# Kernel optimization log

Hardware: AMD Instinct MI355X
Metric: run time of the kernel (lower is better)

The kernel has to match this reference:

```python
import jax, jax.numpy as jnp
import numpy as np

H = 256    # hidden_size
CVQ = 64   # vq_ph_channel
K = 128    # vq_ph_codebook_dim
NL = 5     # num_layers per ConvBlocks
NB = 2     # layers_in_block
KS = 3     # kernel_size


def _ln_c(x, g, b, eps=1e-5):
    # LayerNorm over channel dim of a [B, C, T] tensor
    m = jnp.mean(x, axis=1, keepdims=True)
    v = jnp.mean((x - m) ** 2, axis=1, keepdims=True)
    return (x - m) * jax.lax.rsqrt(v + eps) * g[None, :, None] + b[None, :, None]


def _causal_conv(x, w, b):
    # x [B,Cin,T], w [Cout,Cin,K]; left (causal) padding of K-1
    y = jax.lax.conv_general_dilated(x, w, (1,), [(w.shape[-1] - 1, 0)],
                                     dimension_numbers=('NCH', 'OIH', 'NCH'))
    return y + b[None, :, None]


def _pw(x, w, b):
    # pointwise (kernel-size-1) conv: w [Cout, Cin]
    return jnp.einsum('oi,bit->bot', w, x) + b[None, :, None]


def _conv_blocks(x, mask, ln_g, ln_b, w1, b1, w2, b2, last_g, last_b, post_w, post_b):
    # LeftPadConvBlocks: NL residual blocks x NB sub-blocks of
    # LN -> causal conv (C->2C, k=3) -> *k^-0.5 -> GELU -> 1x1 conv (2C->C), residual + mask
    scale = KS ** -0.5
    for i in range(NL):
        for j in range(NB):
            h = _ln_c(x, ln_g[i, j], ln_b[i, j])
            h = _causal_conv(h, w1[i, j], b1[i, j]) * scale
            h = jax.nn.gelu(h, approximate=False)
            h = _pw(h, w2[i, j], b2[i, j])
            x = (x + h) * mask
    x = _ln_c(x, last_g, last_b) * mask
    x = _causal_conv(x, post_w, post_b) * mask
    return x


def _group_by_segs(h_bct, mel2ph, L):
    # scatter-mean mel frames into phoneme segments; index 0 = padding (dropped)
    h = jnp.swapaxes(h_bct, 1, 2)  # [B, T, H]
    def one(hb, mb):
        s = jnp.zeros((L + 1, hb.shape[-1]), hb.dtype).at[mb].add(hb)
        c = jnp.zeros((L + 1,), hb.dtype).at[mb].add(1.0)
        return s[1:] / jnp.clip(c[1:], 1.0)[:, None]
    g = jax.vmap(one)(h, mel2ph)   # [B, L, H]
    return jnp.swapaxes(g, 1, 2)   # [B, H, L]


def _vq(z, codebook, beta=0.25):
    # EMA-VQ forward math: nearest-codebook lookup + straight-through + commitment loss
    x = jnp.swapaxes(z, 1, 2)                                # [B, T, C]
    d = (jnp.sum(x ** 2, -1, keepdims=True)
         - 2.0 * jnp.einsum('btc,kc->btk', x, codebook)
         + jnp.sum(codebook ** 2, -1))                       # [B, T, K]
    idx = jnp.argmin(d, axis=-1)                             # [B, T]
    q = codebook[idx]                                        # [B, T, C]
    loss = beta * jnp.mean((x - jax.lax.stop_gradient(q)) ** 2)
    q_st = x + jax.lax.stop_gradient(q - x)
    return jnp.swapaxes(q_st, 1, 2), loss, idx


def setup_inputs() -> dict:
    key = jax.random.key(0)
    ks = list(jax.random.split(key, 64))
    it = iter(ks)
    B, T, L = 16, 2048, 512
    f = lambda shape, s: jax.random.normal(next(it), shape, jnp.float32) * s
    inp = {}
    inp['x'] = jax.random.normal(next(it), (B, 80, T), jnp.float32)
    inp['in_nonpadding'] = jnp.ones((B, 1, T), jnp.float32)
    inp['in_mel2ph'] = jnp.sort(jax.random.randint(next(it), (B, T), 1, L + 1), axis=-1)
    inp['ph_nonpadding'] = jnp.ones((B, 1, L), jnp.float32)
    inp['conv_in_w'] = f((H, 80), 0.05)
    inp['conv_in_b'] = jnp.zeros((H,), jnp.float32)
    for p in ('enc', 'pn'):
        inp[p + '_ln_g'] = jnp.ones((NL, NB, H), jnp.float32)
        inp[p + '_ln_b'] = jnp.zeros((NL, NB, H), jnp.float32)
        inp[p + '_w1'] = f((NL, NB, 2 * H, H, KS), 0.03)
        inp[p + '_b1'] = jnp.zeros((NL, NB, 2 * H), jnp.float32)
        inp[p + '_w2'] = f((NL, NB, H, 2 * H), 0.03)
        inp[p + '_b2'] = jnp.zeros((NL, NB, H), jnp.float32)
        inp[p + '_last_g'] = jnp.ones((H,), jnp.float32)
        inp[p + '_last_b'] = jnp.zeros((H,), jnp.float32)
        inp[p + '_post_w'] = f((H, H, KS), 0.03)
        inp[p + '_post_b'] = jnp.zeros((H,), jnp.float32)
    inp['proj_in_w'] = f((CVQ, H), 0.05)
    inp['proj_in_b'] = jnp.zeros((CVQ,), jnp.float32)
    inp['proj_out_w'] = f((H, CVQ), 0.05)
    inp['proj_out_b'] = jnp.zeros((H,), jnp.float32)
    inp['codebook'] = f((K, CVQ), 0.1)
    return inp


def reference(x, in_nonpadding, in_mel2ph, ph_nonpadding,
              conv_in_w, conv_in_b,
              enc_ln_g, enc_ln_b, enc_w1, enc_b1, enc_w2, enc_b2,
              enc_last_g, enc_last_b, enc_post_w, enc_post_b,
              pn_ln_g, pn_ln_b, pn_w1, pn_b1, pn_w2, pn_b2,
              pn_last_g, pn_last_b, pn_post_w, pn_post_b,
              proj_in_w, proj_in_b, proj_out_w, proj_out_b, codebook):
    L = ph_nonpadding.shape[-1]
    h = _pw(x, conv_in_w, conv_in_b) * in_nonpadding                     # ph_conv_in
    h = _conv_blocks(h, in_nonpadding, enc_ln_g, enc_ln_b, enc_w1, enc_b1,
                     enc_w2, enc_b2, enc_last_g, enc_last_b,
                     enc_post_w, enc_post_b) * in_nonpadding             # ph_encoder
    h = _group_by_segs(h, in_mel2ph, L)                                  # [B, H, L]
    h = _conv_blocks(h, ph_nonpadding, pn_ln_g, pn_ln_b, pn_w1, pn_b1,
                     pn_w2, pn_b2, pn_last_g, pn_last_b,
                     pn_post_w, pn_post_b) * ph_nonpadding               # ph_postnet
    z = _pw(h, proj_in_w, proj_in_b)                                     # ph_latents_proj_in
    q, vq_loss, idx = _vq(z, codebook)                                   # VQ
    out = _pw(q, proj_out_w, proj_out_b)                                 # ph_latents_proj_out
    return out, vq_loss, idx
```

## Files before the change

### kernel.cpp

```cpp
#include <hip/hip_runtime.h>
#include <hip/hip_bf16.h>


typedef unsigned short u16;
typedef unsigned int u32;
typedef __attribute__((ext_vector_type(8))) _Float16 f16x8;
typedef __attribute__((ext_vector_type(16))) float f32x16;

#define OUT_LOSS_OFF 2097152
#define OUT_IDX_OFF  2097153

__device__ __forceinline__ void split_f16(float x, u16& h, u16& l) {
    union { _Float16 f; u16 u; } a, b;
    a.f = (_Float16)x;
    float hf = (float)a.f;
    b.f = (_Float16)(x - hf);
    h = a.u; l = b.u;
}

__device__ __forceinline__ void gelu_pack(float v, float bb, u16* GH, u16* GL,
                                          int off) {
    const float ks = 0.5773502691896258f;
    float y = (v + bb) * ks;
    float ge = 0.5f * y * (1.0f + erff(y * 0.7071067811865476f));
// ... 43 lines not shown
        int L = (int)((i >> 3) & 63);
        int nt = (int)((i >> 9) & 7);
        int kb = (int)((i >> 12) & 31);
        int s = (int)(i >> 17);
        int oc = nt * 32 + (L & 31);
        int ic = kb * 16 + ((L >> 5) << 3) + j;
        float v = w[((size_t)s * 256 + oc) * 512 + ic];
        u16 h, l; split_f16(v, h, l);
        BH[i] = h; BL[i] = l;
    }
}

__global__ __launch_bounds__(256) void k_t_wpmf(const float* __restrict__ w,
                                                u16* __restrict__ BH,
                                                u16* __restrict__ BL) {
    int i = blockIdx.x * 256 + threadIdx.x;
    int j = i & 7;
    int L = (i >> 3) & 63;
    int nt = (i >> 9) & 7;
    int kb = (i >> 12) & 15;
    int k3 = i >> 16;
    int oc = nt * 32 + (L & 31);
    int c = kb * 16 + ((L >> 5) << 3) + j;
    float v = w[((size_t)oc * 256 + c) * 3 + k3];
    u16 h, l; split_f16(v, h, l);
    BH[i] = h; BL[i] = l;
}

template <int CIN, int COUT, int CHUNK, bool STATS>
__global__ __launch_bounds__(256) void k_pw(const float* __restrict__ x,
                                            const float* __restrict__ wt,
                                            const float* __restrict__ bias,
                                            const float* __restrict__ mask,
                                            float* __restrict__ y,
                                            float* __restrict__ MM,
                                            float* __restrict__ IV, int T) {
    extern __shared__ float X[];
    constexpr int NG = COUT / CHUNK;
    __shared__ float rs[64 * NG], rs2[64 * NG];
    const int b = blockIdx.y, t0 = blockIdx.x * 64;
    for (int i = threadIdx.x; i < CIN * 64; i += 256) {
        int ci = i >> 6, j = i & 63;
        X[i] = x[((size_t)b * CIN + ci) * T + t0 + j];
    }
    __syncthreads();
    const int tl = threadIdx.x & 63;
    const int g = __builtin_amdgcn_readfirstlane((int)(threadIdx.x >> 6));
    float acc[CHUNK];
#pragma unroll
    for (int o = 0; o < CHUNK; o++) acc[o] = 0.f;
    for (int i = 0; i < CIN; i++) {
        float xv = X[i * 64 + tl];
        const float* wr = wt + (size_t)i * COUT + g * CHUNK;
#pragma unroll
        for (int o = 0; o < CHUNK; o++) acc[o] = fmaf(wr[o], xv, acc[o]);
    }
    float mk = mask ? mask[(size_t)b * T + t0 + tl] : 1.0f;
    float s = 0.f, s2 = 0.f;
#pragma unroll
    for (int o = 0; o < CHUNK; o++) {
        int oc = g * CHUNK + o;
        float val = (acc[o] + bias[oc]) * mk;
        y[((size_t)b * COUT + oc) * T + t0 + tl] = val;
        s += val; s2 += val * val;
    }
    if constexpr (STATS) {
        rs[g * 64 + tl] = s; rs2[g * 64 + tl] = s2;
        __syncthreads();
        if (threadIdx.x < 64) {
            float ss = 0.f, ss2 = 0.f;
#pragma unroll
            for (int gg = 0; gg < NG; gg++) {
                ss += rs[gg * 64 + threadIdx.x];
                ss2 += rs2[gg * 64 + threadIdx.x];
            }
            float m = ss * (1.0f / COUT);
            float var = ss2 * (1.0f / COUT) - m * m;
            MM[(size_t)b * T + t0 + threadIdx.x] = m;
            IV[(size_t)b * T + t0 + threadIdx.x] = 1.0f / sqrtf(var + 1e-5f);
        }
    }
}

template <int M>
__global__ __launch_bounds__(512, 4) void k_sub(
    const float* __restrict__ xin, float* __restrict__ xout,
    const float* __restrict__ MMi, const float* __restrict__ IVi,
    const float* __restrict__ lng, const float* __restrict__ lnb,
    const u16* __restrict__ B1H, const u16* __restrict__ B1L,
    const float* __restrict__ b1,
    const u16* __restrict__ B2H, const u16* __restrict__ B2L,
    const float* __restrict__ b2, const float* __restrict__ mask,
    float* __restrict__ MMo, float* __restrict__ IVo, int T) {
    constexpr int MT = M / 32;
    constexpr int SH = (M + 2) * 264 * 2;
    constexpr int CG = 512 / M;
    constexpr int CPT = 256 / CG;
    __shared__ __align__(16) char smem[2 * SH + 4096];
    u16* LH = (u16*)smem;
    u16* LL = (u16*)(smem + SH);
    u16* GH = (u16*)smem;
    u16* GL = (u16*)(smem + SH);
    float* SOUT = (float*)smem;
    float* rs  = (float*)(smem + 2 * SH);
    float* rs2 = (float*)(smem + 2 * SH + 2048);

    const int tid = threadIdx.x;
    const int b = blockIdx.y, t0 = blockIdx.x * M;
    const size_t xoff = (size_t)b * 256 * T;
    const size_t bT = (size_t)b * T;

    {
        int jj = tid & (M - 1);
        int cg = tid / M;
        int t = t0 - 2 + jj;
        bool ok = (t >= 0);
        float m = ok ? MMi[bT + t] : 0.f;
        float v = ok ? IVi[bT + t] : 0.f;
#pragma unroll
        for (int i = 0; i < CPT; i++) {
            int c = cg + i * CG;
            float xv = ok ? xin[xoff + (size_t)c * T + t] : 0.f;
            float ln = ok ? ((xv - m) * v * lng[c] + lnb[c]) : 0.f;
            u16 h, l; split_f16(ln, h, l);
            LH[jj * 264 + c] = h; LL[jj * 264 + c] = l;
        }
        int j2 = M + (tid >> 8);
        int c2 = tid & 255;
        int t2 = t0 + (M - 2) + (tid >> 8);
        float m2 = MMi[bT + t2], v2 = IVi[bT + t2];
        float x2 = xin[xoff + (size_t)c2 * T + t2];
        float ln2 = (x2 - m2) * v2 * lng[c2] + lnb[c2];
        u16 h2, l2; split_f16(ln2, h2, l2);
        LH[j2 * 264 + c2] = h2; LL[j2 * 264 + c2] = l2;
    }
    __syncthreads();

    const int lane = tid & 63;
    const int w = tid >> 6;
    const int arow = lane & 31;
    const int acol = (lane >> 5) << 3;
    const int thalf = (lane >> 5) << 2;
    const int oc_l = w * 32 + (lane & 31);
    const u16* b1h0 = B1H + (size_t)w * 512 + (size_t)lane * 8;
    const u16* b1l0 = B1L + (size_t)w * 512 + (size_t)lane * 8;
    const u16* b1h1 = B1H + (size_t)(8 + w) * 512 + (size_t)lane * 8;
    const u16* b1l1 = B1L + (size_t)(8 + w) * 512 + (size_t)lane * 8;
    const u16* b2h = B2H + (size_t)w * 512 + (size_t)lane * 8;
    const u16* b2l = B2L + (size_t)w * 512 + (size_t)lane * 8;

    f32x16 c0[MT], c1[MT];
#pragma unroll
    for (int m = 0; m < MT; m++)
#pragma unroll
        for (int r = 0; r < 16; r++) { c0[m][r] = 0.f; c1[m][r] = 0.f; }
    __builtin_amdgcn_s_setprio(1);
#pragma unroll 2
    for (int kk = 0; kk < 48; kk++) {
        int k3 = kk >> 4, kb = kk & 15;
        f16x8 bh0 = *(const f16x8*)(b1h0 + (size_t)kk * 8192);
        f16x8 bl0 = *(const f16x8*)(b1l0 + (size_t)kk * 8192);
        f16x8 bh1 = *(const f16x8*)(b1h1 + (size_t)kk * 8192);
        f16x8 bl1 = *(const f16x8*)(b1l1 + (size_t)kk * 8192);
        f16x8 ah[MT], al[MT];
#pragma unroll
        for (int m = 0; m < MT; m++) {
            int ao = (m * 32 + arow + k3) * 264 + kb * 16 + acol;
            ah[m] = *(const f16x8*)&LH[ao];
            al[m] = *(const f16x8*)&LL[ao];
        }
#pragma unroll
        for (int m = 0; m < MT; m++) {
            c0[m] = __builtin_amdgcn_mfma_f32_32x32x16_f16(ah[m], bh0, c0[m], 0, 0, 0);
            c1[m] = __builtin_amdgcn_mfma_f32_32x32x16_f16(ah[m], bh1, c1[m], 0, 0, 0);
        }
#pragma unroll
        for (int m = 0; m < MT; m++) {
            c0[m] = __builtin_amdgcn_mfma_f32_32x32x16_f16(ah[m], bl0, c0[m], 0, 0, 0);
            c1[m] = __builtin_amdgcn_mfma_f32_32x32x16_f16(ah[m], bl1, c1[m], 0, 0, 0);
        }
#pragma unroll
        for (int m = 0; m < MT; m++) {
            c0[m] = __builtin_amdgcn_mfma_f32_32x32x16_f16(al[m], bh0, c0[m], 0, 0, 0);
            c1[m] = __builtin_amdgcn_mfma_f32_32x32x16_f16(al[m], bh1, c1[m], 0, 0, 0);
        }
    }
    __builtin_amdgcn_s_setprio(0);
    __syncthreads();

    {
        float bb = b1[oc_l];
#pragma unroll
        for (int m = 0; m < MT; m++)
#pragma unroll
            for (int r = 0; r < 16; r++) {
                int trow = m * 32 + thalf + ((r >> 2) << 3) + (r & 3);
                gelu_pack(c0[m][r], bb, GH, GL, trow * 264 + oc_l);
            }
    }
    __syncthreads();

#pragma unroll
    for (int m = 0; m < MT; m++)
#pragma unroll
        for (int r = 0; r < 16; r++) c0[m][r] = 0.f;
    __builtin_amdgcn_s_setprio(1);
#pragma unroll 2
    for (int i = 0; i < 16; i++) {
        f16x8 bh2 = *(const f16x8*)(b2h + (size_t)i * 4096);
        f16x8 bl2 = *(const f16x8*)(b2l + (size_t)i * 4096);
        f16x8 gh[MT], gl[MT];
#pragma unroll
        for (int m = 0; m < MT; m++) {
            int go = (m * 32 + arow) * 264 + i * 16 + acol;
            gh[m] = *(const f16x8*)&GH[go];
            gl[m] = *(const f16x8*)&GL[go];
        }
#pragma unroll
        for (int m = 0; m < MT; m++)
            c0[m] = __builtin_amdgcn_mfma_f32_32x32x16_f16(gh[m], bh2, c0[m], 0, 0, 0);
#pragma unroll
        for (int m = 0; m < MT; m++)
            c0[m] = __builtin_amdgcn_mfma_f32_32x32x16_f16(gh[m], bl2, c0[m], 0, 0, 0);
#pragma unroll
        for (int m = 0; m < MT; m++)
            c0[m] = __builtin_amdgcn_mfma_f32_32x32x16_f16(gl[m], bh2, c0[m], 0, 0, 0);
    }
    __builtin_amdgcn_s_setprio(0);
    __syncthreads();

    {
        float bb = b1[256 + oc_l];
#pragma unroll
        for (int m = 0; m < MT; m++)
#pragma unroll
            for (int r = 0; r < 16; r++) {
                int trow = m * 32 + thalf + ((r >> 2) << 3) + (r & 3);
                gelu_pack(c1[m][r], bb, GH, GL, trow * 264 + oc_l);
            }
    }
    __syncthreads();

    __builtin_amdgcn_s_setprio(1);
#pragma unroll 2
    for (int i = 0; i < 16; i++) {
        f16x8 bh2 = *(const f16x8*)(b2h + (size_t)(16 + i) * 4096);
        f16x8 bl2 = *(const f16x8*)(b2l + (size_t)(16 + i) * 4096);
        f16x8 gh[MT], gl[MT];
#pragma unroll
        for (int m = 0; m < MT; m++) {
            int go = (m * 32 + arow) * 264 + i * 16 + acol;
            gh[m] = *(const f16x8*)&GH[go];
            gl[m] = *(const f16x8*)&GL[go];
        }
#pragma unroll
        for (int m = 0; m < MT; m++)
            c0[m] = __builtin_amdgcn_mfma_f32_32x32x16_f16(gh[m], bh2, c0[m], 0, 0, 0);
#pragma unroll
        for (int m = 0; m < MT; m++)
            c0[m] = __builtin_amdgcn_mfma_f32_32x32x16_f16(gh[m], bl2, c0[m], 0, 0, 0);
#pragma unroll
        for (int m = 0; m < MT; m++)
            c0[m] = __builtin_amdgcn_mfma_f32_32x32x16_f16(gl[m], bh2, c0[m], 0, 0, 0);
    }
    __builtin_amdgcn_s_setprio(0);
    __syncthreads();

#pragma unroll
    for (int m = 0; m < MT; m++)
#pragma unroll
        for (int r = 0; r < 16; r++) {
            int trow = m * 32 + thalf + ((r >> 2) << 3) + (r & 3);
            SOUT[trow * 260 + oc_l] = c0[m][r];
        }
    __syncthreads();
    {
        int t = tid & (M - 1), cg = tid / M;
        float mk = mask[bT + t0 + t];
        float s = 0.f, s2 = 0.f;
#pragma unroll
        for (int i = 0; i < CPT; i++) {
            int c = cg * CPT + i;
            size_t adr = xoff + (size_t)c * T + t0 + t;
            float val = (xin[adr] + SOUT[t * 260 + c] + b2[c]) * mk;
            xout[adr] = val;
            s += val; s2 += val * val;
        }
        rs[tid] = s; rs2[tid] = s2;
    }
    __syncthreads();
    if (tid < M) {
        float ss = 0.f, ss2 = 0.f;
#pragma unroll
        for (int k = 0; k < CG; k++) {
            ss += rs[k * M + tid]; ss2 += rs2[k * M + tid];
        }
        float m = ss * (1.0f / 256.0f);
        float var = ss2 * (1.0f / 256.0f) - m * m;
        MMo[bT + t0 + tid] = m;
        IVo[bT + t0 + tid] = 1.0f / sqrtf(var + 1e-5f);
    }
}

__global__ __launch_bounds__(1024, 4) void k_sub16(
    const float* __restrict__ xin, float* __restrict__ xout,
    const float* __restrict__ MMi, const float* __restrict__ IVi,
    const float* __restrict__ lng, const float* __restrict__ lnb,
    const u16* __restrict__ B1H, const u16* __restrict__ B1L,
    const float* __restrict__ b1,
    const u16* __restrict__ B2H, const u16* __restrict__ B2L,
    const float* __restrict__ b2, const float* __restrict__ mask,
    float* __restrict__ MMo, float* __restrict__ IVo, int T) {
    __shared__ __align__(16) char smem[76800];
    u16* LH = (u16*)smem;
    u16* LL = (u16*)(smem + 17952);
    u16* GH = (u16*)smem;
    u16* GL = (u16*)(smem + 34304);
    float* SOUT  = (float*)smem;
    float* SOUT2 = (float*)(smem + 34304);
    float* rs  = (float*)(smem + 68608);
    float* rs2 = (float*)(smem + 72704);

    const int tid = threadIdx.x;
    const int b = blockIdx.y, t0 = blockIdx.x * 32;
    const size_t xoff = (size_t)b * 256 * T;
    const size_t bT = (size_t)b * T;

    {
        int jj = tid & 31;
        int cg = tid >> 5;
        int t = t0 - 2 + jj;
        bool ok = (t >= 0);
        float m = ok ? MMi[bT + t] : 0.f;
        float v = ok ? IVi[bT + t] : 0.f;
#pragma unroll
        for (int i = 0; i < 8; i++) {
            int c = cg + i * 32;
            float xv = ok ? xin[xoff + (size_t)c * T + t] : 0.f;
            float ln = ok ? ((xv - m) * v * lng[c] + lnb[c]) : 0.f;
            u16 h, l; split_f16(ln, h, l);
            LH[jj * 264 + c] = h; LL[jj * 264 + c] = l;
        }
        if (tid < 512) {
            int j2 = 32 + (tid >> 8);
            int c2 = tid & 255;
            int t2 = t0 + 30 + (tid >> 8);
            float ln2 = (xin[xoff + (size_t)c2 * T + t2] - MMi[bT + t2]) *
                        IVi[bT + t2] * lng[c2] + lnb[c2];
            u16 h2, l2; split_f16(ln2, h2, l2);
            LH[j2 * 264 + c2] = h2; LL[j2 * 264 + c2] = l2;
        }
    }
    __syncthreads();

    const int lane = tid & 63;
    const int w = tid >> 6;
    const int arow = lane & 31;
    const int acol = (lane >> 5) << 3;
    const int thalf = (lane >> 5) << 2;
    const int oc_l = w * 32 + (lane & 31);
    const u16* b1h = B1H + (size_t)w * 512 + (size_t)lane * 8;
    const u16* b1l = B1L + (size_t)w * 512 + (size_t)lane * 8;

    f32x16 cc;
#pragma unroll
    for (int r = 0; r < 16; r++) cc[r] = 0.f;
    __builtin_amdgcn_s_setprio(1);
#pragma unroll 4
    for (int kk = 0; kk < 48; kk++) {
        int k3 = kk >> 4, kb = kk & 15;
        int ao = (arow + k3) * 264 + kb * 16 + acol;
        f16x8 ah = *(const f16x8*)&LH[ao];
        f16x8 al = *(const f16x8*)&LL[ao];
        f16x8 bh = *(const f16x8*)(b1h + (size_t)kk * 8192);
        f16x8 bl = *(const f16x8*)(b1l + (size_t)kk * 8192);
        cc = __builtin_amdgcn_mfma_f32_32x32x16_f16(ah, bh, cc, 0, 0, 0);
        cc = __builtin_amdgcn_mfma_f32_32x32x16_f16(ah, bl, cc, 0, 0, 0);
        cc = __builtin_amdgcn_mfma_f32_32x32x16_f16(al, bh, cc, 0, 0, 0);
    }
    __builtin_amdgcn_s_setprio(0);
    __syncthreads();

    {
        float bb = b1[oc_l];
// ... 323 lines not shown
    (void)in_sizes; (void)n_in; (void)out_size; (void)ws_size;
    const float* x          = (const float*)d_in[0];
    const float* in_np      = (const float*)d_in[1];
    const int*   mel2ph     = (const int*)d_in[2];
    const float* ph_np      = (const float*)d_in[3];
    const float* conv_in_w  = (const float*)d_in[4];
    const float* conv_in_b  = (const float*)d_in[5];
    const float* e_ln_g = (const float*)d_in[6];
    const float* e_ln_b = (const float*)d_in[7];
    const float* e_w1   = (const float*)d_in[8];
    const float* e_b1   = (const float*)d_in[9];
    const float* e_w2   = (const float*)d_in[10];
    const float* e_b2   = (const float*)d_in[11];
    const float* e_lg   = (const float*)d_in[12];
    const float* e_lb   = (const float*)d_in[13];
    const float* e_pw   = (const float*)d_in[14];
    const float* e_pb   = (const float*)d_in[15];
    const float* p_ln_g = (const float*)d_in[16];
    const float* p_ln_b = (const float*)d_in[17];
    const float* p_w1   = (const float*)d_in[18];
    const float* p_b1   = (const float*)d_in[19];
    const float* p_w2   = (const float*)d_in[20];
    const float* p_b2   = (const float*)d_in[21];
    const float* p_lg   = (const float*)d_in[22];
    const float* p_lb   = (const float*)d_in[23];
    const float* p_pw   = (const float*)d_in[24];
    const float* p_pb   = (const float*)d_in[25];
    const float* proj_in_w  = (const float*)d_in[26];
    const float* proj_in_b  = (const float*)d_in[27];
    const float* proj_out_w = (const float*)d_in[28];
    const float* proj_out_b = (const float*)d_in[29];
    const float* codebook   = (const float*)d_in[30];
    float* out = (float*)d_out;

    float* ws = (float*)d_ws;
    float* A      = ws;
    float* Bb     = A + 8388608;
    float* CINT   = Bb + 8388608;
    float* PINT   = CINT + 20480;
    float* POUTT  = PINT + 16384;
    float* Z      = POUTT + 16384;
    float* MM0    = Z + 524288;
    float* IV0    = MM0 + 32768;
    float* MM1    = IV0 + 32768;
    float* IV1    = MM1 + 32768;
    int*   CNT    = (int*)(IV1 + 32768);
    int*   IDX    = CNT + 8192;
    float* LOSS   = (float*)(IDX + 8192);
    u16*   BH1E   = (u16*)(LOSS + 64);
    u16*   BL1E   = BH1E + 3932160;
    u16*   BH1P   = BL1E + 3932160;
    u16*   BL1P   = BH1P + 3932160;
    u16*   BH2E   = BL1P + 3932160;
    u16*   BL2E   = BH2E + 1310720;
    u16*   BH2P   = BL2E + 1310720;
    u16*   BL2P   = BH2P + 1310720;
    u16*   PH_E   = BL2P + 1310720;
    u16*   PL_E   = PH_E + 196608;
    u16*   PH_P   = PL_E + 196608;
    u16*   PL_P   = PH_P + 196608;

    k_t_w1mf<<<dim3(4096), dim3(256), 0, stream>>>(e_w1, BH1E, BL1E, 10);
    k_t_w1mf<<<dim3(4096), dim3(256), 0, stream>>>(p_w1, BH1P, BL1P, 10);
    k_t_w2mf<<<dim3(2048), dim3(256), 0, stream>>>(e_w2, BH2E, BL2E, 10);
    k_t_w2mf<<<dim3(2048), dim3(256), 0, stream>>>(p_w2, BH2P, BL2P, 10);
    k_t_wpmf<<<dim3(768),  dim3(256), 0, stream>>>(e_pw, PH_E, PL_E);
    k_t_wpmf<<<dim3(768),  dim3(256), 0, stream>>>(p_pw, PH_P, PL_P);
    k_t_mat  <<<dim3(80),  dim3(256), 0, stream>>>(conv_in_w, CINT, 1, 256, 80);
    k_t_mat  <<<dim3(64),  dim3(256), 0, stream>>>(proj_in_w, PINT, 1, 64, 256);
    k_t_mat  <<<dim3(64),  dim3(256), 0, stream>>>(proj_out_w, POUTT, 1, 256, 64);

    const size_t sm_scat = 256 * 65 * sizeof(float) + 64 * sizeof(int);

    k_pw<80, 256, 64, true><<<dim3(32, 16), dim3(256), 80 * 64 * 4, stream>>>(
        x, CINT, conv_in_b, in_np, A, MM0, IV0, 2048);

    float* cur = A;
    float* nxt = Bb;
    for (int s = 0; s < 10; s++) {
        float* mi = (s & 1) ? MM1 : MM0;
        float* vi = (s & 1) ? IV1 : IV0;
        float* mo = (s & 1) ? MM0 : MM1;
        float* vo = (s & 1) ? IV0 : IV1;
        k_sub<64><<<dim3(32, 16), dim3(512), 0, stream>>>(
            cur, nxt, mi, vi, e_ln_g + s * 256, e_ln_b + s * 256,
            BH1E + (size_t)s * 393216, BL1E + (size_t)s * 393216, e_b1 + s * 512,
            BH2E + (size_t)s * 131072, BL2E + (size_t)s * 131072, e_b2 + s * 256,
            in_np, mo, vo, 2048);
        float* t = cur; cur = nxt; nxt = t;
    }
    k_lnc<64><<<dim3(32, 16), dim3(512), 0, stream>>>(
        cur, nxt, MM0, IV0, e_lg, e_lb, PH_E, PL_E, e_pb, in_np, 2048);

    hipMemsetAsync(A, 0, (size_t)2097152 * 4, stream);
    hipMemsetAsync(LOSS, 0, 4, stream);
    k_counts<<<dim3(16), dim3(256), 0, stream>>>(mel2ph, CNT);
    k_scatter<<<dim3(32, 16), dim3(256), sm_scat, stream>>>(Bb, mel2ph, A);
    k_postprep<<<dim3(16), dim3(512), 0, stream>>>(A, CNT, MM0, IV0);

    cur = A; nxt = Bb;
    for (int s = 0; s < 10; s++) {
        float* mi = (s & 1) ? MM1 : MM0;
        float* vi = (s & 1) ? IV1 : IV0;
        float* mo = (s & 1) ? MM0 : MM1;
        float* vo = (s & 1) ? IV0 : IV1;
        k_sub16<<<dim3(16, 16), dim3(1024), 0, stream>>>(
            cur, nxt, mi, vi, p_ln_g + s * 256, p_ln_b + s * 256,
            BH1P + (size_t)s * 393216, BL1P + (size_t)s * 393216, p_b1 + s * 512,
            BH2P + (size_t)s * 131072, BL2P + (size_t)s * 131072, p_b2 + s * 256,
            ph_np, mo, vo, 512);
        float* t = cur; cur = nxt; nxt = t;
    }
    k_lnc<32><<<dim3(16, 16), dim3(512), 0, stream>>>(
        cur, nxt, MM0, IV0, p_lg, p_lb, PH_P, PL_P, p_pb, ph_np, 512);

    k_pw<256, 64, 16, false><<<dim3(8, 16), dim3(256), 256 * 64 * 4, stream>>>(
        Bb, PINT, proj_in_b, nullptr, Z, nullptr, nullptr, 512);

    k_vq<<<dim3(64), dim3(256), 0, stream>>>(Z, codebook, IDX, out, LOSS);
    k_loss<<<dim3(1), dim3(64), 0, stream>>>(LOSS, out);
    k_projout<<<dim3(8, 16), dim3(256), 0, stream>>>(codebook, IDX, POUTT,
                                                     proj_out_b, out);
}
```

Baseline: 2.061 ms.

## Pair two time tiles per block with staggered phases to overlap stages

Replaces the 512-thread encoder sub-block kernel with a 1024-thread kernel holding two independent 64-frame tiles in separate shared-memory halves. The two tiles run their stages offset by one step, so one half's staging, GELU packing or epilogue overlaps the other half's MFMA conv loops within the same CU. The aim is to hide memory and VALU phases behind matrix work. In exchange, shared memory per block roughly doubles to about 144 KB, which limits occupancy, and every phase boundary now needs a barrier across 1024 threads.

```diff
diff --git a/kernel.cpp b/kernel.cpp
--- a/kernel.cpp
+++ b/kernel.cpp
@@ -149,8 +149,7 @@
     }
 }
 
-template <int M>
-__global__ __launch_bounds__(512, 4) void k_sub(
+__global__ __launch_bounds__(1024, 4) void k_sub2(
     const float* __restrict__ xin, float* __restrict__ xout,
     const float* __restrict__ MMi, const float* __restrict__ IVi,
     const float* __restrict__ lng, const float* __restrict__ lnb,
@@ -159,49 +158,22 @@
     const u16* __restrict__ B2H, const u16* __restrict__ B2L,
     const float* __restrict__ b2, const float* __restrict__ mask,
     float* __restrict__ MMo, float* __restrict__ IVo, int T) {
-    constexpr int MT = M / 32;
-    constexpr int SH = (M + 2) * 264 * 2;
-    constexpr int CG = 512 / M;
-    constexpr int CPT = 256 / CG;
-    __shared__ __align__(16) char smem[2 * SH + 4096];
-    u16* LH = (u16*)smem;
-    u16* LL = (u16*)(smem + SH);
-    u16* GH = (u16*)smem;
-    u16* GL = (u16*)(smem + SH);
-    float* SOUT = (float*)smem;
-    float* rs  = (float*)(smem + 2 * SH);
-    float* rs2 = (float*)(smem + 2 * SH + 2048);
-
-    const int tid = threadIdx.x;
-    const int b = blockIdx.y, t0 = blockIdx.x * M;
+    __shared__ __align__(16) char smem[147584];
+    const int grp = (int)(threadIdx.x >> 9);
+    const int tid = (int)(threadIdx.x & 511);
+    char* basep = smem + (size_t)grp * 73792;
+    u16* LH = (u16*)basep;
+    u16* LL = (u16*)(basep + 34848);
+    u16* GH = (u16*)basep;
+    u16* GL = (u16*)(basep + 34848);
+    float* SO = (float*)basep;
+    float* rs  = (float*)(basep + 69696);
+    float* rs2 = (float*)(basep + 71744);
+
+    const int b = blockIdx.y;
+    const int t0 = blockIdx.x * 128 + grp * 64;
     const size_t xoff = (size_t)b * 256 * T;
     const size_t bT = (size_t)b * T;
-
-    {
-        int jj = tid & (M - 1);
-        int cg = tid / M;
-        int t = t0 - 2 + jj;
-        bool ok = (t >= 0);
-        float m = ok ? MMi[bT + t] : 0.f;
-        float v = ok ? IVi[bT + t] : 0.f;
-#pragma unroll
-        for (int i = 0; i < CPT; i++) {
-            int c = cg + i * CG;
-            float xv = ok ? xin[xoff + (size_t)c * T + t] : 0.f;
-            float ln = ok ? ((xv - m) * v * lng[c] + lnb[c]) : 0.f;
-            u16 h, l; split_f16(ln, h, l);
-            LH[jj * 264 + c] = h; LL[jj * 264 + c] = l;
-        }
-        int j2 = M + (tid >> 8);
-        int c2 = tid & 255;
-        int t2 = t0 + (M - 2) + (tid >> 8);
-        float m2 = MMi[bT + t2], v2 = IVi[bT + t2];
-        float x2 = xin[xoff + (size_t)c2 * T + t2];
-        float ln2 = (x2 - m2) * v2 * lng[c2] + lnb[c2];
-        u16 h2, l2; split_f16(ln2, h2, l2);
-        LH[j2 * 264 + c2] = h2; LL[j2 * 264 + c2] = l2;
-    }
-    __syncthreads();
 
     const int lane = tid & 63;
     const int w = tid >> 6;
@@ -216,157 +188,193 @@
     const u16* b2h = B2H + (size_t)w * 512 + (size_t)lane * 8;
     const u16* b2l = B2L + (size_t)w * 512 + (size_t)lane * 8;
 
-    f32x16 c0[MT], c1[MT];
-#pragma unroll
-    for (int m = 0; m < MT; m++)
-#pragma unroll
-        for (int r = 0; r < 16; r++) { c0[m][r] = 0.f; c1[m][r] = 0.f; }
-    __builtin_amdgcn_s_setprio(1);
-#pragma unroll 2
-    for (int kk = 0; kk < 48; kk++) {
-        int k3 = kk >> 4, kb = kk & 15;
-        f16x8 bh0 = *(const f16x8*)(b1h0 + (size_t)kk * 8192);
-        f16x8 bl0 = *(const f16x8*)(b1l0 + (size_t)kk * 8192);
-        f16x8 bh1 = *(const f16x8*)(b1h1 + (size_t)kk * 8192);
-        f16x8 bl1 = *(const f16x8*)(b1l1 + (size_t)kk * 8192);
-        f16x8 ah[MT], al[MT];
-#pragma unroll
-        for (int m = 0; m < MT; m++) {
-            int ao = (m * 32 + arow + k3) * 264 + kb * 16 + acol;
-            ah[m] = *(const f16x8*)&LH[ao];
-            al[m] = *(const f16x8*)&LL[ao];
-        }
-#pragma unroll
-        for (int m = 0; m < MT; m++) {
-            c0[m] = __builtin_amdgcn_mfma_f32_32x32x16_f16(ah[m], bh0, c0[m], 0, 0, 0);
-            c1[m] = __builtin_amdgcn_mfma_f32_32x32x16_f16(ah[m], bh1, c1[m], 0, 0, 0);
-        }
-#pragma unroll
-        for (int m = 0; m < MT; m++) {
-            c0[m] = __builtin_amdgcn_mfma_f32_32x32x16_f16(ah[m], bl0, c0[m], 0, 0, 0);
-            c1[m] = __builtin_amdgcn_mfma_f32_32x32x16_f16(ah[m], bl1, c1[m], 0, 0, 0);
-        }
-#pragma unroll
-        for (int m = 0; m < MT; m++) {
-            c0[m] = __builtin_amdgcn_mfma_f32_32x32x16_f16(al[m], bh0, c0[m], 0, 0, 0);
-            c1[m] = __builtin_amdgcn_mfma_f32_32x32x16_f16(al[m], bh1, c1[m], 0, 0, 0);
-        }
-    }
-    __builtin_amdgcn_s_setprio(0);
-    __syncthreads();
-
-    {
-        float bb = b1[oc_l];
-#pragma unroll
-        for (int m = 0; m < MT; m++)
-#pragma unroll
-            for (int r = 0; r < 16; r++) {
-                int trow = m * 32 + thalf + ((r >> 2) << 3) + (r & 3);
-                gelu_pack(c0[m][r], bb, GH, GL, trow * 264 + oc_l);
-            }
-    }
-    __syncthreads();
-
-#pragma unroll
-    for (int m = 0; m < MT; m++)
-#pragma unroll
-        for (int r = 0; r < 16; r++) c0[m][r] = 0.f;
-    __builtin_amdgcn_s_setprio(1);
-#pragma unroll 2
-    for (int i = 0; i < 16; i++) {
-        f16x8 bh2 = *(const f16x8*)(b2h + (size_t)i * 4096);
-        f16x8 bl2 = *(const f16x8*)(b2l + (size_t)i * 4096);
-        f16x8 gh[MT], gl[MT];
-#pragma unroll
-        for (int m = 0; m < MT; m++) {
-            int go = (m * 32 + arow) * 264 + i * 16 + acol;
-            gh[m] = *(const f16x8*)&GH[go];
-            gl[m] = *(const f16x8*)&GL[go];
-        }
-#pragma unroll
-        for (int m = 0; m < MT; m++)
-            c0[m] = __builtin_amdgcn_mfma_f32_32x32x16_f16(gh[m], bh2, c0[m], 0, 0, 0);
-#pragma unroll
-        for (int m = 0; m < MT; m++)
-            c0[m] = __builtin_amdgcn_mfma_f32_32x32x16_f16(gh[m], bl2, c0[m], 0, 0, 0);
-#pragma unroll
-        for (int m = 0; m < MT; m++)
-            c0[m] = __builtin_amdgcn_mfma_f32_32x32x16_f16(gl[m], bh2, c0[m], 0, 0, 0);
-    }
-    __builtin_amdgcn_s_setprio(0);
-    __syncthreads();
-
-    {
-        float bb = b1[256 + oc_l];
-#pragma unroll
-        for (int m = 0; m < MT; m++)
-#pragma unroll
-            for (int r = 0; r < 16; r++) {
-                int trow = m * 32 + thalf + ((r >> 2) << 3) + (r & 3);
-                gelu_pack(c1[m][r], bb, GH, GL, trow * 264 + oc_l);
-            }
-    }
-    __syncthreads();
-
-    __builtin_amdgcn_s_setprio(1);
-#pragma unroll 2
-    for (int i = 0; i < 16; i++) {
-        f16x8 bh2 = *(const f16x8*)(b2h + (size_t)(16 + i) * 4096);
-        f16x8 bl2 = *(const f16x8*)(b2l + (size_t)(16 + i) * 4096);
-        f16x8 gh[MT], gl[MT];
-#pragma unroll
-        for (int m = 0; m < MT; m++) {
-            int go = (m * 32 + arow) * 264 + i * 16 + acol;
-            gh[m] = *(const f16x8*)&GH[go];
-            gl[m] = *(const f16x8*)&GL[go];
-        }
-#pragma unroll
-        for (int m = 0; m < MT; m++)
-            c0[m] = __builtin_amdgcn_mfma_f32_32x32x16_f16(gh[m], bh2, c0[m], 0, 0, 0);
-#pragma unroll
-        for (int m = 0; m < MT; m++)
-            c0[m] = __builtin_amdgcn_mfma_f32_32x32x16_f16(gh[m], bl2, c0[m], 0, 0, 0);
-#pragma unroll
-        for (int m = 0; m < MT; m++)
-            c0[m] = __builtin_amdgcn_mfma_f32_32x32x16_f16(gl[m], bh2, c0[m], 0, 0, 0);
-    }
-    __builtin_amdgcn_s_setprio(0);
-    __syncthreads();
-
-#pragma unroll
-    for (int m = 0; m < MT; m++)
-#pragma unroll
-        for (int r = 0; r < 16; r++) {
-            int trow = m * 32 + thalf + ((r >> 2) << 3) + (r & 3);
-            SOUT[trow * 260 + oc_l] = c0[m][r];
-        }
-    __syncthreads();
-    {
-        int t = tid & (M - 1), cg = tid / M;
-        float mk = mask[bT + t0 + t];
-        float s = 0.f, s2 = 0.f;
-#pragma unroll
-        for (int i = 0; i < CPT; i++) {
-            int c = cg * CPT + i;
-            size_t adr = xoff + (size_t)c * T + t0 + t;
-            float val = (xin[adr] + SOUT[t * 260 + c] + b2[c]) * mk;
-            xout[adr] = val;
-            s += val; s2 += val * val;
-        }
-        rs[tid] = s; rs2[tid] = s2;
-    }
-    __syncthreads();
-    if (tid < M) {
-        float ss = 0.f, ss2 = 0.f;
-#pragma unroll
-        for (int k = 0; k < CG; k++) {
-            ss += rs[k * M + tid]; ss2 += rs2[k * M + tid];
-        }
-        float m = ss * (1.0f / 256.0f);
-        float var = ss2 * (1.0f / 256.0f) - m * m;
-        MMo[bT + t0 + tid] = m;
-        IVo[bT + t0 + tid] = 1.0f / sqrtf(var + 1e-5f);
-    }
+    f32x16 c0[2], c1[2];
+
+#define PH_STAGE do {                                                         \
+        int jj = tid & 63;                                                    \
+        int cg = tid >> 6;                                                    \
+        int t = t0 - 2 + jj;                                                  \
+        bool ok = (t >= 0);                                                   \
+        float m = ok ? MMi[bT + t] : 0.f;                                     \
+        float v = ok ? IVi[bT + t] : 0.f;                                     \
+        _Pragma("unroll")                                                     \
+        for (int i = 0; i < 32; i++) {                                        \
+            int c = cg + i * 8;                                               \
+            float xv = ok ? xin[xoff + (size_t)c * T + t] : 0.f;              \
+            float ln = ok ? ((xv - m) * v * lng[c] + lnb[c]) : 0.f;           \
+            u16 h, l; split_f16(ln, h, l);                                    \
+            LH[jj * 264 + c] = h; LL[jj * 264 + c] = l;                       \
+        }                                                                     \
+        int j2 = 64 + (tid >> 8);                                             \
+        int c2 = tid & 255;                                                   \
+        int t2 = t0 + 62 + (tid >> 8);                                        \
+        float m2 = MMi[bT + t2], v2 = IVi[bT + t2];                           \
+        float x2 = xin[xoff + (size_t)c2 * T + t2];                           \
+        float ln2 = (x2 - m2) * v2 * lng[c2] + lnb[c2];                       \
+        u16 h2, l2; split_f16(ln2, h2, l2);                                   \
+        LH[j2 * 264 + c2] = h2; LL[j2 * 264 + c2] = l2;                       \
+    } while (0)
+
+#define PH_CONV1 do {                                                         \
+        _Pragma("unroll")                                                     \
+        for (int m = 0; m < 2; m++)                                           \
+            _Pragma("unroll")                                                 \
+            for (int r = 0; r < 16; r++) { c0[m][r] = 0.f; c1[m][r] = 0.f; }  \
+        __builtin_amdgcn_s_setprio(1);                                        \
+        _Pragma("unroll 2")                                                   \
+        for (int kk = 0; kk < 48; kk++) {                                     \
+            int k3 = kk >> 4, kb = kk & 15;                                   \
+            f16x8 bh0 = *(const f16x8*)(b1h0 + (size_t)kk * 8192);            \
+            f16x8 bl0 = *(const f16x8*)(b1l0 + (size_t)kk * 8192);            \
+            f16x8 bh1 = *(const f16x8*)(b1h1 + (size_t)kk * 8192);            \
+            f16x8 bl1 = *(const f16x8*)(b1l1 + (size_t)kk * 8192);            \
+            f16x8 ah[2], al[2];                                               \
+            _Pragma("unroll")                                                 \
+            for (int m = 0; m < 2; m++) {                                     \
+                int ao = (m * 32 + arow + k3) * 264 + kb * 16 + acol;         \
+                ah[m] = *(const f16x8*)&LH[ao];                               \
+                al[m] = *(const f16x8*)&LL[ao];                               \
+            }                                                                 \
+            _Pragma("unroll")                                                 \
+            for (int m = 0; m < 2; m++) {                                     \
+                c0[m] = __builtin_amdgcn_mfma_f32_32x32x16_f16(ah[m], bh0, c0[m], 0, 0, 0); \
+                c1[m] = __builtin_amdgcn_mfma_f32_32x32x16_f16(ah[m], bh1, c1[m], 0, 0, 0); \
+            }                                                                 \
+            _Pragma("unroll")                                                 \
+            for (int m = 0; m < 2; m++) {                                     \
+                c0[m] = __builtin_amdgcn_mfma_f32_32x32x16_f16(ah[m], bl0, c0[m], 0, 0, 0); \
+                c1[m] = __builtin_amdgcn_mfma_f32_32x32x16_f16(ah[m], bl1, c1[m], 0, 0, 0); \
+            }                                                                 \
+            _Pragma("unroll")                                                 \
+            for (int m = 0; m < 2; m++) {                                     \
+                c0[m] = __builtin_amdgcn_mfma_f32_32x32x16_f16(al[m], bh0, c0[m], 0, 0, 0); \
+                c1[m] = __builtin_amdgcn_mfma_f32_32x32x16_f16(al[m], bh1, c1[m], 0, 0, 0); \
+            }                                                                 \
+        }                                                                     \
+        __builtin_amdgcn_s_setprio(0);                                        \
+    } while (0)
+
+#define PH_PACK0 do {                                                         \
+        float bb = b1[oc_l];                                                  \
+        _Pragma("unroll")                                                     \
+        for (int m = 0; m < 2; m++)                                           \
+            _Pragma("unroll")                                                 \
+            for (int r = 0; r < 16; r++) {                                    \
+                int trow = m * 32 + thalf + ((r >> 2) << 3) + (r & 3);        \
+                gelu_pack(c0[m][r], bb, GH, GL, trow * 264 + oc_l);           \
+            }                                                                 \
+    } while (0)
+
+#define PH_PACK1 do {                                                         \
+        float bb = b1[256 + oc_l];                                            \
+        _Pragma("unroll")                                                     \
+        for (int m = 0; m < 2; m++)                                           \
+            _Pragma("unroll")                                                 \
+            for (int r = 0; r < 16; r++) {                                    \
+                int trow = m * 32 + thalf + ((r >> 2) << 3) + (r & 3);        \
+                gelu_pack(c1[m][r], bb, GH, GL, trow * 264 + oc_l);           \
+            }                                                                 \
+    } while (0)
+
+#define PH_CONV2(IOFF, ZERO) do {                                             \
+        if (ZERO) {                                                           \
+            _Pragma("unroll")                                                 \
+            for (int m = 0; m < 2; m++)                                       \
+                _Pragma("unroll")                                             \
+                for (int r = 0; r < 16; r++) c0[m][r] = 0.f;                  \
+        }                                                                     \
+        __builtin_amdgcn_s_setprio(1);                                        \
+        _Pragma("unroll 2")                                                   \
+        for (int i = 0; i < 16; i++) {                                        \
+            f16x8 bh2 = *(const f16x8*)(b2h + (size_t)(IOFF + i) * 4096);     \
+            f16x8 bl2 = *(const f16x8*)(b2l + (size_t)(IOFF + i) * 4096);     \
+            f16x8 gh[2], gl[2];                                               \
+            _Pragma("unroll")                                                 \
+            for (int m = 0; m < 2; m++) {                                     \
+                int go = (m * 32 + arow) * 264 + i * 16 + acol;               \
+                gh[m] = *(const f16x8*)&GH[go];                               \
+                gl[m] = *(const f16x8*)&GL[go];                               \
+            }                                                                 \
+            _Pragma("unroll")                                                 \
+            for (int m = 0; m < 2; m++)                                       \
+                c0[m] = __builtin_amdgcn_mfma_f32_32x32x16_f16(gh[m], bh2, c0[m], 0, 0, 0); \
+            _Pragma("unroll")                                                 \
+            for (int m = 0; m < 2; m++)                                       \
+                c0[m] = __builtin_amdgcn_mfma_f32_32x32x16_f16(gh[m], bl2, c0[m], 0, 0, 0); \
+            _Pragma("unroll")                                                 \
+            for (int m = 0; m < 2; m++)                                       \
+                c0[m] = __builtin_amdgcn_mfma_f32_32x32x16_f16(gl[m], bh2, c0[m], 0, 0, 0); \
+        }                                                                     \
+        __builtin_amdgcn_s_setprio(0);                                        \
+    } while (0)
+
+#define PH_SOUT do {                                                          \
+        _Pragma("unroll")                                                     \
+        for (int m = 0; m < 2; m++)                                           \
+            _Pragma("unroll")                                                 \
+            for (int r = 0; r < 16; r++) {                                    \
+                int trow = m * 32 + thalf + ((r >> 2) << 3) + (r & 3);        \
+                SO[trow * 260 + oc_l] = c0[m][r];                             \
+            }                                                                 \
+    } while (0)
+
+#define PH_EPI do {                                                           \
+        int t = tid & 63, cg = tid >> 6;                                      \
+        float mk = mask[bT + t0 + t];                                         \
+        float s = 0.f, s2 = 0.f;                                              \
+        _Pragma("unroll")                                                     \
+        for (int i = 0; i < 32; i++) {                                        \
+            int c = cg * 32 + i;                                              \
+            size_t adr = xoff + (size_t)c * T + t0 + t;                       \
+            float val = (xin[adr] + SO[t * 260 + c] + b2[c]) * mk;            \
+            xout[adr] = val;                                                  \
+            s += val; s2 += val * val;                                        \
+        }                                                                     \
+        rs[tid] = s; rs2[tid] = s2;                                           \
+    } while (0)
+
+#define PH_STATS do {                                                         \
+        if (tid < 64) {                                                       \
+            float ss = 0.f, ss2 = 0.f;                                        \
+            _Pragma("unroll")                                                 \
+            for (int k = 0; k < 8; k++) {                                     \
+                ss += rs[k * 64 + tid]; ss2 += rs2[k * 64 + tid];             \
+            }                                                                 \
+            float m = ss * (1.0f / 256.0f);                                   \
+            float var = ss2 * (1.0f / 256.0f) - m * m;                        \
+            MMo[bT + t0 + tid] = m;                                           \
+            IVo[bT + t0 + tid] = 1.0f / sqrtf(var + 1e-5f);                   \
+        }                                                                     \
+    } while (0)
+
+    if (grp == 0) PH_STAGE;
+    __syncthreads();
+    if (grp == 0) PH_CONV1; else PH_STAGE;
+    __syncthreads();
+    if (grp == 0) PH_PACK0; else PH_CONV1;
+    __syncthreads();
+    if (grp == 0) PH_CONV2(0, true); else PH_PACK0;
+    __syncthreads();
+    if (grp == 0) PH_PACK1; else PH_CONV2(0, true);
+    __syncthreads();
+    if (grp == 0) PH_CONV2(16, false); else PH_PACK1;
+    __syncthreads();
+    if (grp == 0) PH_SOUT; else PH_CONV2(16, false);
+    __syncthreads();
+    if (grp == 0) { PH_EPI; } else PH_SOUT;
+    __syncthreads();
+    if (grp == 0) { PH_STATS; } else { PH_EPI; }
+    __syncthreads();
+    if (grp == 1) PH_STATS;
+
+#undef PH_STAGE
+#undef PH_CONV1
+#undef PH_PACK0
+#undef PH_PACK1
+#undef PH_CONV2
+#undef PH_SOUT
+#undef PH_EPI
+#undef PH_STATS
 }
 
 __global__ __launch_bounds__(1024, 4) void k_sub16(
@@ -856,7 +864,7 @@
         float* vi = (s & 1) ? IV1 : IV0;
         float* mo = (s & 1) ? MM0 : MM1;
         float* vo = (s & 1) ? IV0 : IV1;
-        k_sub<64><<<dim3(32, 16), dim3(512), 0, stream>>>(
+        k_sub2<<<dim3(16, 16), dim3(1024), 0, stream>>>(
             cur, nxt, mi, vi, e_ln_g + s * 256, e_ln_b + s * 256,
             BH1E + (size_t)s * 393216, BL1E + (size_t)s * 393216, e_b1 + s * 512,
             BH2E + (size_t)s * 131072, BL2E + (size_t)s * 131072, e_b2 + s * 256,
```

Measured after the change: 2.122 ms. 3.0% more time.

## Enlarge encoder sublayer tile to 128 timesteps with 1024-thread blocks

Applied to the files above, without the earlier changes.

Replaces the templated 64-timestep sublayer kernel with a dedicated 128-timestep version run by 16 waves per block. Each wave now computes one 32-channel slice of the causal-conv GEMM, so every weight fragment fetched from global memory serves twice as many timesteps and the grid is halved. The cost is that only half the waves take part in the pointwise GEMM stages and the GELU stages are serialized between wave groups. LDS use rises to about 145 KB, which limits residency to one block per CU.

```diff
diff --git a/kernel.cpp b/kernel.cpp
--- a/kernel.cpp
+++ b/kernel.cpp
@@ -149,8 +149,7 @@
     }
 }
 
-template <int M>
-__global__ __launch_bounds__(512, 4) void k_sub(
+__global__ __launch_bounds__(1024, 4) void k_sub128(
     const float* __restrict__ xin, float* __restrict__ xout,
     const float* __restrict__ MMi, const float* __restrict__ IVi,
     const float* __restrict__ lng, const float* __restrict__ lnb,
@@ -159,47 +158,45 @@
     const u16* __restrict__ B2H, const u16* __restrict__ B2L,
     const float* __restrict__ b2, const float* __restrict__ mask,
     float* __restrict__ MMo, float* __restrict__ IVo, int T) {
-    constexpr int MT = M / 32;
-    constexpr int SH = (M + 2) * 264 * 2;
-    constexpr int CG = 512 / M;
-    constexpr int CPT = 256 / CG;
-    __shared__ __align__(16) char smem[2 * SH + 4096];
+    __shared__ __align__(16) char smem[145472];
     u16* LH = (u16*)smem;
-    u16* LL = (u16*)(smem + SH);
+    u16* LL = (u16*)(smem + 68640);
     u16* GH = (u16*)smem;
-    u16* GL = (u16*)(smem + SH);
+    u16* GL = (u16*)(smem + 68640);
     float* SOUT = (float*)smem;
-    float* rs  = (float*)(smem + 2 * SH);
-    float* rs2 = (float*)(smem + 2 * SH + 2048);
+    float* rs  = (float*)(smem + 137280);
+    float* rs2 = (float*)(smem + 141376);
 
     const int tid = threadIdx.x;
-    const int b = blockIdx.y, t0 = blockIdx.x * M;
+    const int b = blockIdx.y, t0 = blockIdx.x * 128;
     const size_t xoff = (size_t)b * 256 * T;
     const size_t bT = (size_t)b * T;
 
     {
-        int jj = tid & (M - 1);
-        int cg = tid / M;
+        int jj = tid & 127;
+        int cg = tid >> 7;
         int t = t0 - 2 + jj;
         bool ok = (t >= 0);
         float m = ok ? MMi[bT + t] : 0.f;
         float v = ok ? IVi[bT + t] : 0.f;
 #pragma unroll
-        for (int i = 0; i < CPT; i++) {
-            int c = cg + i * CG;
+        for (int i = 0; i < 32; i++) {
+            int c = cg + i * 8;
             float xv = ok ? xin[xoff + (size_t)c * T + t] : 0.f;
             float ln = ok ? ((xv - m) * v * lng[c] + lnb[c]) : 0.f;
             u16 h, l; split_f16(ln, h, l);
             LH[jj * 264 + c] = h; LL[jj * 264 + c] = l;
         }
-        int j2 = M + (tid >> 8);
-        int c2 = tid & 255;
-        int t2 = t0 + (M - 2) + (tid >> 8);
-        float m2 = MMi[bT + t2], v2 = IVi[bT + t2];
-        float x2 = xin[xoff + (size_t)c2 * T + t2];
-        float ln2 = (x2 - m2) * v2 * lng[c2] + lnb[c2];
-        u16 h2, l2; split_f16(ln2, h2, l2);
-        LH[j2 * 264 + c2] = h2; LL[j2 * 264 + c2] = l2;
+        if (tid < 512) {
+            int j2 = 128 + (tid >> 8);
+            int c2 = tid & 255;
+            int t2 = t0 + 126 + (tid >> 8);
+            float m2 = MMi[bT + t2], v2 = IVi[bT + t2];
+            float x2 = xin[xoff + (size_t)c2 * T + t2];
+            float ln2 = (x2 - m2) * v2 * lng[c2] + lnb[c2];
+            u16 h2, l2; split_f16(ln2, h2, l2);
+            LH[j2 * 264 + c2] = h2; LL[j2 * 264 + c2] = l2;
+        }
     }
     __syncthreads();
 
@@ -208,146 +205,144 @@
     const int arow = lane & 31;
     const int acol = (lane >> 5) << 3;
     const int thalf = (lane >> 5) << 2;
-    const int oc_l = w * 32 + (lane & 31);
-    const u16* b1h0 = B1H + (size_t)w * 512 + (size_t)lane * 8;
-    const u16* b1l0 = B1L + (size_t)w * 512 + (size_t)lane * 8;
-    const u16* b1h1 = B1H + (size_t)(8 + w) * 512 + (size_t)lane * 8;
-    const u16* b1l1 = B1L + (size_t)(8 + w) * 512 + (size_t)lane * 8;
-    const u16* b2h = B2H + (size_t)w * 512 + (size_t)lane * 8;
-    const u16* b2l = B2L + (size_t)w * 512 + (size_t)lane * 8;
-
-    f32x16 c0[MT], c1[MT];
-#pragma unroll
-    for (int m = 0; m < MT; m++)
-#pragma unroll
-        for (int r = 0; r < 16; r++) { c0[m][r] = 0.f; c1[m][r] = 0.f; }
+    const u16* b1h = B1H + (size_t)w * 512 + (size_t)lane * 8;
+    const u16* b1l = B1L + (size_t)w * 512 + (size_t)lane * 8;
+    const u16* b2h = B2H + (size_t)(w & 7) * 512 + (size_t)lane * 8;
+    const u16* b2l = B2L + (size_t)(w & 7) * 512 + (size_t)lane * 8;
+
+    f32x16 c0[4];
+#pragma unroll
+    for (int m = 0; m < 4; m++)
+#pragma unroll
+        for (int r = 0; r < 16; r++) c0[m][r] = 0.f;
     __builtin_amdgcn_s_setprio(1);
 #pragma unroll 2
     for (int kk = 0; kk < 48; kk++) {
         int k3 = kk >> 4, kb = kk & 15;
-        f16x8 bh0 = *(const f16x8*)(b1h0 + (size_t)kk * 8192);
-        f16x8 bl0 = *(const f16x8*)(b1l0 + (size_t)kk * 8192);
-        f16x8 bh1 = *(const f16x8*)(b1h1 + (size_t)kk * 8192);
-        f16x8 bl1 = *(const f16x8*)(b1l1 + (size_t)kk * 8192);
-        f16x8 ah[MT], al[MT];
-#pragma unroll
-        for (int m = 0; m < MT; m++) {
+        f16x8 bh = *(const f16x8*)(b1h + (size_t)kk * 8192);
+        f16x8 bl = *(const f16x8*)(b1l + (size_t)kk * 8192);
+        f16x8 ah[4], al[4];
+#pragma unroll
+        for (int m = 0; m < 4; m++) {
             int ao = (m * 32 + arow + k3) * 264 + kb * 16 + acol;
             ah[m] = *(const f16x8*)&LH[ao];
             al[m] = *(const f16x8*)&LL[ao];
         }
 #pragma unroll
-        for (int m = 0; m < MT; m++) {
-            c0[m] = __builtin_amdgcn_mfma_f32_32x32x16_f16(ah[m], bh0, c0[m], 0, 0, 0);
-            c1[m] = __builtin_amdgcn_mfma_f32_32x32x16_f16(ah[m], bh1, c1[m], 0, 0, 0);
-        }
-#pragma unroll
-        for (int m = 0; m < MT; m++) {
-            c0[m] = __builtin_amdgcn_mfma_f32_32x32x16_f16(ah[m], bl0, c0[m], 0, 0, 0);
-            c1[m] = __builtin_amdgcn_mfma_f32_32x32x16_f16(ah[m], bl1, c1[m], 0, 0, 0);
-        }
-#pragma unroll
-        for (int m = 0; m < MT; m++) {
-            c0[m] = __builtin_amdgcn_mfma_f32_32x32x16_f16(al[m], bh0, c0[m], 0, 0, 0);
-            c1[m] = __builtin_amdgcn_mfma_f32_32x32x16_f16(al[m], bh1, c1[m], 0, 0, 0);
-        }
+        for (int m = 0; m < 4; m++)
+            c0[m] = __builtin_amdgcn_mfma_f32_32x32x16_f16(ah[m], bh, c0[m], 0, 0, 0);
+#pragma unroll
+        for (int m = 0; m < 4; m++)
+            c0[m] = __builtin_amdgcn_mfma_f32_32x32x16_f16(ah[m], bl, c0[m], 0, 0, 0);
+#pragma unroll
+        for (int m = 0; m < 4; m++)
+            c0[m] = __builtin_amdgcn_mfma_f32_32x32x16_f16(al[m], bh, c0[m], 0, 0, 0);
     }
     __builtin_amdgcn_s_setprio(0);
     __syncthreads();
 
-    {
-        float bb = b1[oc_l];
-#pragma unroll
-        for (int m = 0; m < MT; m++)
+    if (w < 8) {
+        int oc = w * 32 + (lane & 31);
+        float bb = b1[oc];
+#pragma unroll
+        for (int m = 0; m < 4; m++)
 #pragma unroll
             for (int r = 0; r < 16; r++) {
                 int trow = m * 32 + thalf + ((r >> 2) << 3) + (r & 3);
-                gelu_pack(c0[m][r], bb, GH, GL, trow * 264 + oc_l);
+                gelu_pack(c0[m][r], bb, GH, GL, trow * 264 + oc);
             }
     }
     __syncthreads();
 
-#pragma unroll
-    for (int m = 0; m < MT; m++)
-#pragma unroll
-        for (int r = 0; r < 16; r++) c0[m][r] = 0.f;
-    __builtin_amdgcn_s_setprio(1);
+    if (w < 8) {
+#pragma unroll
+        for (int m = 0; m < 4; m++)
+#pragma unroll
+            for (int r = 0; r < 16; r++) c0[m][r] = 0.f;
+        __builtin_amdgcn_s_setprio(1);
 #pragma unroll 2
-    for (int i = 0; i < 16; i++) {
-        f16x8 bh2 = *(const f16x8*)(b2h + (size_t)i * 4096);
-        f16x8 bl2 = *(const f16x8*)(b2l + (size_t)i * 4096);
-        f16x8 gh[MT], gl[MT];
-#pragma unroll
-        for (int m = 0; m < MT; m++) {
-            int go = (m * 32 + arow) * 264 + i * 16 + acol;
-            gh[m] = *(const f16x8*)&GH[go];
-            gl[m] = *(const f16x8*)&GL[go];
-        }
-#pragma unroll
-        for (int m = 0; m < MT; m++)
-            c0[m] = __builtin_amdgcn_mfma_f32_32x32x16_f16(gh[m], bh2, c0[m], 0, 0, 0);
-#pragma unroll
-        for (int m = 0; m < MT; m++)
-            c0[m] = __builtin_amdgcn_mfma_f32_32x32x16_f16(gh[m], bl2, c0[m], 0, 0, 0);
-#pragma unroll
-        for (int m = 0; m < MT; m++)
-            c0[m] = __builtin_amdgcn_mfma_f32_32x32x16_f16(gl[m], bh2, c0[m], 0, 0, 0);
-    }
-    __builtin_amdgcn_s_setprio(0);
-    __syncthreads();
-
-    {
-        float bb = b1[256 + oc_l];
-#pragma unroll
-        for (int m = 0; m < MT; m++)
+        for (int i = 0; i < 16; i++) {
+            f16x8 bh2 = *(const f16x8*)(b2h + (size_t)i * 4096);
+            f16x8 bl2 = *(const f16x8*)(b2l + (size_t)i * 4096);
+            f16x8 gh[4], gl[4];
+#pragma unroll
+            for (int m = 0; m < 4; m++) {
+                int go = (m * 32 + arow) * 264 + i * 16 + acol;
+                gh[m] = *(const f16x8*)&GH[go];
+                gl[m] = *(const f16x8*)&GL[go];
+            }
+#pragma unroll
+            for (int m = 0; m < 4; m++)
+                c0[m] = __builtin_amdgcn_mfma_f32_32x32x16_f16(gh[m], bh2, c0[m], 0, 0, 0);
+#pragma unroll
+            for (int m = 0; m < 4; m++)
+                c0[m] = __builtin_amdgcn_mfma_f32_32x32x16_f16(gh[m], bl2, c0[m], 0, 0, 0);
+#pragma unroll
+            for (int m = 0; m < 4; m++)
+                c0[m] = __builtin_amdgcn_mfma_f32_32x32x16_f16(gl[m], bh2, c0[m], 0, 0, 0);
+        }
+        __builtin_amdgcn_s_setprio(0);
+    }
+    __syncthreads();
+
+    if (w >= 8) {
+        int ocp = (w - 8) * 32 + (lane & 31);
+        float bb = b1[256 + ocp];
+#pragma unroll
+        for (int m = 0; m < 4; m++)
 #pragma unroll
             for (int r = 0; r < 16; r++) {
                 int trow = m * 32 + thalf + ((r >> 2) << 3) + (r & 3);
-                gelu_pack(c1[m][r], bb, GH, GL, trow * 264 + oc_l);
+                gelu_pack(c0[m][r], bb, GH, GL, trow * 264 + ocp);
             }
     }
     __syncthreads();
 
-    __builtin_amdgcn_s_setprio(1);
+    if (w < 8) {
+        __builtin_amdgcn_s_setprio(1);
 #pragma unroll 2
-    for (int i = 0; i < 16; i++) {
-        f16x8 bh2 = *(const f16x8*)(b2h + (size_t)(16 + i) * 4096);
-        f16x8 bl2 = *(const f16x8*)(b2l + (size_t)(16 + i) * 4096);
-        f16x8 gh[MT], gl[MT];
-#pragma unroll
-        for (int m = 0; m < MT; m++) {
-            int go = (m * 32 + arow) * 264 + i * 16 + acol;
-            gh[m] = *(const f16x8*)&GH[go];
-            gl[m] = *(const f16x8*)&GL[go];
-        }
-#pragma unroll
-        for (int m = 0; m < MT; m++)
-            c0[m] = __builtin_amdgcn_mfma_f32_32x32x16_f16(gh[m], bh2, c0[m], 0, 0, 0);
-#pragma unroll
-        for (int m = 0; m < MT; m++)
-            c0[m] = __builtin_amdgcn_mfma_f32_32x32x16_f16(gh[m], bl2, c0[m], 0, 0, 0);
-#pragma unroll
-        for (int m = 0; m < MT; m++)
-            c0[m] = __builtin_amdgcn_mfma_f32_32x32x16_f16(gl[m], bh2, c0[m], 0, 0, 0);
-    }
-    __builtin_amdgcn_s_setprio(0);
-    __syncthreads();
-
-#pragma unroll
-    for (int m = 0; m < MT; m++)
-#pragma unroll
-        for (int r = 0; r < 16; r++) {
-            int trow = m * 32 + thalf + ((r >> 2) << 3) + (r & 3);
-            SOUT[trow * 260 + oc_l] = c0[m][r];
-        }
+        for (int i = 0; i < 16; i++) {
+            f16x8 bh2 = *(const f16x8*)(b2h + (size_t)(16 + i) * 4096);
+            f16x8 bl2 = *(const f16x8*)(b2l + (size_t)(16 + i) * 4096);
+            f16x8 gh[4], gl[4];
+#pragma unroll
+            for (int m = 0; m < 4; m++) {
+                int go = (m * 32 + arow) * 264 + i * 16 + acol;
+                gh[m] = *(const f16x8*)&GH[go];
+                gl[m] = *(const f16x8*)&GL[go];
+            }
+#pragma unroll
+            for (int m = 0; m < 4; m++)
+                c0[m] = __builtin_amdgcn_mfma_f32_32x32x16_f16(gh[m], bh2, c0[m], 0, 0, 0);
+#pragma unroll
+            for (int m = 0; m < 4; m++)
+                c0[m] = __builtin_amdgcn_mfma_f32_32x32x16_f16(gh[m], bl2, c0[m], 0, 0, 0);
+#pragma unroll
+            for (int m = 0; m < 4; m++)
+                c0[m] = __builtin_amdgcn_mfma_f32_32x32x16_f16(gl[m], bh2, c0[m], 0, 0, 0);
+        }
+        __builtin_amdgcn_s_setprio(0);
+    }
+    __syncthreads();
+
+    if (w < 8) {
+        int oc = w * 32 + (lane & 31);
+#pragma unroll
+        for (int m = 0; m < 4; m++)
+#pragma unroll
+            for (int r = 0; r < 16; r++) {
+                int trow = m * 32 + thalf + ((r >> 2) << 3) + (r & 3);
+                SOUT[trow * 260 + oc] = c0[m][r];
+            }
+    }
     __syncthreads();
     {
-        int t = tid & (M - 1), cg = tid / M;
+        int t = tid & 127, cg = tid >> 7;
         float mk = mask[bT + t0 + t];
         float s = 0.f, s2 = 0.f;
 #pragma unroll
-        for (int i = 0; i < CPT; i++) {
-            int c = cg * CPT + i;
+        for (int i = 0; i < 32; i++) {
+            int c = cg * 32 + i;
             size_t adr = xoff + (size_t)c * T + t0 + t;
             float val = (xin[adr] + SOUT[t * 260 + c] + b2[c]) * mk;
             xout[adr] = val;
@@ -356,11 +351,11 @@
         rs[tid] = s; rs2[tid] = s2;
     }
     __syncthreads();
-    if (tid < M) {
+    if (tid < 128) {
         float ss = 0.f, ss2 = 0.f;
 #pragma unroll
-        for (int k = 0; k < CG; k++) {
-            ss += rs[k * M + tid]; ss2 += rs2[k * M + tid];
+        for (int k = 0; k < 8; k++) {
+            ss += rs[k * 128 + tid]; ss2 += rs2[k * 128 + tid];
         }
         float m = ss * (1.0f / 256.0f);
         float var = ss2 * (1.0f / 256.0f) - m * m;
@@ -856,7 +851,7 @@
         float* vi = (s & 1) ? IV1 : IV0;
         float* mo = (s & 1) ? MM0 : MM1;
         float* vo = (s & 1) ? IV0 : IV1;
-        k_sub<64><<<dim3(32, 16), dim3(512), 0, stream>>>(
+        k_sub128<<<dim3(16, 16), dim3(1024), 0, stream>>>(
             cur, nxt, mi, vi, e_ln_g + s * 256, e_ln_b + s * 256,
             BH1E + (size_t)s * 393216, BL1E + (size_t)s * 393216, e_b1 + s * 512,
             BH2E + (size_t)s * 131072, BL2E + (size_t)s * 131072, e_b2 + s * 256,
```

Measured after the change: 2.087 ms. No clear change (+1.3%).
